# Optimization experiments

Measured on AMD Instinct MI355X. Metric: run time of the kernel, lower is better.

## Reference

```python
import jax, jax.numpy as jnp
import numpy as np
from jax import lax

B, C, H, W = 2, 256, 64, 64
CI = C // 2           # inter_channels = 128
CH = CI // 2          # key/query channels = 64
EPS = 1e-5


def conv1x1(x, w, b):
    # x: [B,C,H,W], w: [O,C], b: [O]
    return jnp.einsum('oc,bchw->bohw', w, x) + b[None, :, None, None]


def bn(x, g, be, m, v):
    inv = (g / jnp.sqrt(v + EPS))[None, :, None, None]
    return (x - m[None, :, None, None]) * inv + be[None, :, None, None]


def setup_inputs() -> dict:
    key = jax.random.key(0)
    ks = jax.random.split(key, 40)
    r = lambda i, shape, sc=0.05: jax.random.normal(ks[i], shape, dtype=jnp.float32) * sc
    u = lambda i, shape: jax.random.uniform(ks[i], shape, dtype=jnp.float32, minval=0.5, maxval=1.5)
    return {
        'q': jax.random.normal(ks[0], (B, C, H, W), dtype=jnp.float32),
        's': jax.random.normal(ks[1], (B, C, H, W), dtype=jnp.float32),
        'scale': jnp.full((1,), 0.3, dtype=jnp.float32),
        'w_v': r(2, (CI, C)), 'b_v': r(3, (CI,)),
        'w_k1': r(4, (CH, C)), 'b_k1': r(5, (CH,)),
        'w_q1': r(6, (CH, C)), 'b_q1': r(7, (CH,)),
        'w_k2': r(8, (CH, C)), 'b_k2': r(9, (CH,)),
        'w_q2': r(10, (CH, C)), 'b_q2': r(11, (CH,)),
        'w_ts': r(12, (CI, C)), 'b_ts': r(13, (CI,)),
        'g_ts': u(14, (CI,)), 'be_ts': r(15, (CI,)), 'm_ts': r(16, (CI,)), 'v_ts': u(17, (CI,)),
        'w_tq': r(18, (CI, C)), 'b_tq': r(19, (CI,)),
        'g_tq': u(20, (CI,)), 'be_tq': r(21, (CI,)), 'm_tq': r(22, (CI,)), 'v_tq': u(23, (CI,)),
        'w_cat': r(24, (CI, 2 * CI, 3, 3)),
        'g_cat': u(25, (CI,)), 'be_cat': r(26, (CI,)), 'm_cat': r(27, (CI,)), 'v_cat': u(28, (CI,)),
    }


def reference(q, s, scale, w_v, b_v, w_k1, b_k1, w_q1, b_q1, w_k2, b_k2, w_q2, b_q2,
              w_ts, b_ts, g_ts, be_ts, m_ts, v_ts,
              w_tq, b_tq, g_tq, be_tq, m_tq, v_tq,
              w_cat, g_cat, be_cat, m_cat, v_cat):
    b_, _, h, w = q.shape
    n = h * w
    # values: [B, N, CI]
    v_q = conv1x1(q, w_v, b_v).reshape(b_, CI, n).transpose(0, 2, 1)
    v_s = conv1x1(s, w_v, b_v).reshape(b_, CI, n).transpose(0, 2, 1)
    # concatenated keys/queries: [B, CI, N]
    k_x = jnp.concatenate([conv1x1(q, w_k1, b_k1), conv1x1(s, w_k2, b_k2)], axis=1).reshape(b_, CI, n)
    q_x = jnp.concatenate([conv1x1(q, w_q1, b_q1), conv1x1(s, w_q2, b_q2)], axis=1).reshape(b_, CI, n)
    # affinity: [B, N, N]
    A_s = jnp.einsum('bcn,bcm->bnm', k_x, q_x)
    attn_s = jax.nn.softmax(A_s, axis=-1)
    attn_q = jax.nn.softmax(jnp.transpose(A_s, (0, 2, 1)), axis=-1)
    # p_s: [B, N, CI] -> [B, CI, H, W]
    p_s = jnp.einsum('bnm,bmc->bnc', attn_s, v_s).transpose(0, 2, 1).reshape(b_, CI, h, w)
    s_t = bn(conv1x1(s, w_ts, b_ts), g_ts, be_ts, m_ts, v_ts)
    q_t = bn(conv1x1(q, w_tq, b_tq), g_tq, be_tq, m_tq, v_tq)
    E_s = scale[0] * p_s + s_t
    q_s_ = jnp.einsum('bnm,bmc->bnc', attn_q, v_q).transpose(0, 2, 1).reshape(b_, CI, h, w)
    E_q = scale[0] * q_s_ + q_t
    cat = jnp.concatenate([E_q, E_s], axis=1)
    conv = lax.conv_general_dilated(cat, w_cat, (1, 1), 'SAME',
                                    dimension_numbers=('NCHW', 'OIHW', 'NCHW'))
    cpam = jax.nn.relu(bn(conv, g_cat, be_cat, m_cat, v_cat))
    return (cpam, E_q, E_s)
```

## Files before the change

### kernel.cpp

```cpp
#include <hip/hip_runtime.h>
#include <hip/hip_bf16.h>

#define NPIX 4096
#define NCH  256
#define CI   128
#define EPS  1e-5f
#define SOFF 20.0f

typedef unsigned short u16;
typedef __attribute__((ext_vector_type(8))) short short8;
typedef __attribute__((ext_vector_type(4))) float f32x4;

__device__ __forceinline__ float bfu2f(u16 u) {
    union { unsigned int i; float f; } x; x.i = ((unsigned int)u) << 16; return x.f;
}
__device__ __forceinline__ u16 f2bfu(float f) {
    union { float ff; unsigned int i; } x; x.ff = f;
    unsigned int r = x.i + 0x7FFFu + ((x.i >> 16) & 1u);
    return (u16)(r >> 16);
}

__device__ __forceinline__ void gload16(const u16* g, u16* l) {
    __builtin_amdgcn_global_load_lds(
        (const __attribute__((address_space(1))) unsigned int*)g,
        (__attribute__((address_space(3))) unsigned int*)l,
        16, 0, 0);
}

__global__ __launch_bounds__(256) void prep_kernel(
    const float* __restrict__ w_v,
    const float* __restrict__ w_k1, const float* __restrict__ w_q1,
    const float* __restrict__ w_k2, const float* __restrict__ w_q2,
    const float* __restrict__ w_ts, const float* __restrict__ w_tq,
    u16* __restrict__ Wbf,
    const float* __restrict__ w_cat, u16* __restrict__ wT)
{
    const int bx = blockIdx.x;
    if (bx < 768) {
        int idx = bx * 256 + threadIdx.x;
        int src = idx / 98304;
        int r   = idx - src * 98304;
        int o   = r >> 8, c = r & 255;
        float v;
        if (o < 128)      v = w_v[(size_t)o * 256 + c];
        else if (o < 192) v = (src ? w_k2 : w_k1)[(size_t)(o - 128) * 256 + c];
        else if (o < 256) v = (src ? w_q2 : w_q1)[(size_t)(o - 192) * 256 + c];
        else              v = (src ? w_ts : w_tq)[(size_t)(o - 256) * 256 + c];
        Wbf[idx] = f2bfu(v);
    } else {
        int co = bx - 768;
        const float* srcb = w_cat + (size_t)co * 2304;
        u16* dstb = wT + (size_t)co * 2304;
        for (int t = threadIdx.x; t < 2304; t += 256) {
            int ic = t / 9, tap = t - ic * 9;
            dstb[tap * 256 + ic] = f2bfu(srcb[t]);
        }
    }
}

__global__ __launch_bounds__(256) void proj2_kernel(
    const float* __restrict__ xq, const float* __restrict__ xs,
    const u16* __restrict__ Wbf,
    const float* __restrict__ b_v,
    const float* __restrict__ b_k1, const float* __restrict__ b_q1,
    const float* __restrict__ b_k2, const float* __restrict__ b_q2,
    const float* __restrict__ b_ts, const float* __restrict__ g_ts,
    const float* __restrict__ be_ts, const float* __restrict__ m_ts,
    const float* __restrict__ v_ts,
    const float* __restrict__ b_tq, const float* __restrict__ g_tq,
    const float* __restrict__ be_tq, const float* __restrict__ m_tq,
    const float* __restrict__ v_tq,
    u16* __restrict__ kT, u16* __restrict__ qT,
    u16* __restrict__ vq, u16* __restrict__ vs,
    u16* __restrict__ tq, u16* __restrict__ ts)
{
    __shared__ u16 Xs[64 * 264];
    __shared__ u16 KQ[64 * 136];

    const int tid  = threadIdx.x;
    const int lane = tid & 63;
    const int wid  = tid >> 6;
    const int l16  = lane & 15;
    const int quad = lane >> 4;

    const int n0  = blockIdx.x * 64;
    const int bz  = blockIdx.z;
    const int b   = bz >> 1, src = bz & 1;

    const float* xg = (src ? xs : xq) + (size_t)b * NCH * NPIX + n0;
    #pragma unroll
    for (int k0 = 0; k0 < 64; k0 += 16) {
        float v[16];
        #pragma unroll
        for (int k = 0; k < 16; ++k) {
            int idx = tid + (k0 + k) * 256;
            int c = idx >> 6, n = idx & 63;
            v[k] = xg[(size_t)c * NPIX + n];
        }
        #pragma unroll
        for (int k = 0; k < 16; ++k) {
            int idx = tid + (k0 + k) * 256;
            int c = idx >> 6, n = idx & 63;
            Xs[n * 264 + c] = f2bfu(v[k]);
        }
    }
    __syncthreads();

    const u16* W = Wbf + (size_t)src * 384 * 256;
    const int o0w = wid * 96;
    const float* bk = src ? b_k2 : b_k1;
    const float* bq = src ? b_q2 : b_q1;
    const float* bt = src ? b_ts : b_tq;

    f32x4 acc[24];
    #pragma unroll
    for (int ot = 0; ot < 6; ++ot) {
        int ob = o0w + ot * 16 + quad * 4;
        const float* bp;
        if (ob < 128)      bp = b_v + ob;
        else if (ob < 192) bp = bk + (ob - 128);
        else if (ob < 256) bp = bq + (ob - 192);
        else               bp = bt + (ob - 256);
        float4 b4 = *(const float4*)bp;
        f32x4 iv = (f32x4){b4.x, b4.y, b4.z, b4.w};
        #pragma unroll
        for (int pt = 0; pt < 4; ++pt) acc[ot * 4 + pt] = iv;
    }

    #pragma unroll
    for (int kc = 0; kc < 8; ++kc) {
        short8 bfr[4];
        #pragma unroll
        for (int pt = 0; pt < 4; ++pt)
            bfr[pt] = *(const short8*)&Xs[(pt * 16 + l16) * 264 + kc * 32 + quad * 8];
        #pragma unroll
        for (int ot = 0; ot < 6; ++ot) {
            short8 a = *(const short8*)&W[(size_t)(o0w + ot * 16 + l16) * 256 + kc * 32 + quad * 8];
            #pragma unroll
            for (int pt = 0; pt < 4; ++pt)
                acc[ot * 4 + pt] = __builtin_amdgcn_mfma_f32_16x16x32_bf16(a, bfr[pt], acc[ot * 4 + pt], 0, 0, 0);
        }
    }

    #pragma unroll
    for (int ot = 0; ot < 6; ++ot) {
        int ob = o0w + ot * 16;
        #pragma unroll
        for (int pt = 0; pt < 4; ++pt) {
            int px = pt * 16 + l16;
            f32x4 v4 = acc[ot * 4 + pt];
            if (ob < 128) {
                u16* dst = src ? vs : vq;
                #pragma unroll
                for (int r = 0; r < 4; ++r)
                    dst[((size_t)b * CI + ob + quad * 4 + r) * NPIX + n0 + px] = f2bfu(v4[r]);
            } else if (ob < 256) {
                int colb = (ob < 192) ? (ob - 128) : (64 + ob - 192);
                #pragma unroll
                for (int r = 0; r < 4; ++r)
                    KQ[px * 136 + colb + quad * 4 + r] = f2bfu(v4[r]);
            } else {
                const float* g  = src ? g_ts  : g_tq;
                const float* be = src ? be_ts : be_tq;
                const float* mm = src ? m_ts  : m_tq;
                const float* vv = src ? v_ts  : v_tq;
                u16* dst = src ? ts : tq;
                #pragma unroll
                for (int r = 0; r < 4; ++r) {
                    int oc = ob - 256 + quad * 4 + r;
                    float inv = g[oc] * rsqrtf(vv[oc] + EPS);
                    dst[((size_t)b * CI + oc) * NPIX + n0 + px] =
                        f2bfu((v4[r] - mm[oc]) * inv + be[oc]);
                }
            }
        }
    }
    __syncthreads();

    const int chb = src ? 64 : 0;
    #pragma unroll
    for (int u = 0; u < 4; ++u) {
        int idx = tid + u * 256;
        int px = idx >> 4, oct = idx & 15;
        uint4 val = *(const uint4*)&KQ[px * 136 + oct * 8];
        if (oct < 8)
            *(uint4*)&kT[((size_t)b * NPIX + n0 + px) * CI + chb + oct * 8] = val;
        else
            *(uint4*)&qT[((size_t)b * NPIX + n0 + px) * CI + chb + (oct - 8) * 8] = val;
    }
}

#define AKS_OFF 0
#define AVT_OFF 16384
#define APS_OFF 32768
#define ASMEM_U16 37376

__global__ __launch_bounds__(256) void attn_kernel(
    const u16* __restrict__ kT, const u16* __restrict__ qT,
    const u16* __restrict__ vq, const u16* __restrict__ vs,
    u16* __restrict__ Opart, float* __restrict__ Lpart, int nseg)
{
    __shared__ __align__(16) u16 smem[ASMEM_U16];
    u16* Ps = smem + APS_OFF;

    const int tid  = threadIdx.x;
    const int lane = tid & 63;
    const int wid  = tid >> 6;
    const int l16  = lane & 15;
    const int quad = lane >> 4;
    const int strip = wid * 16;

    const int nt = blockIdx.x;
    const int n0 = nt * 64;
    const int at = blockIdx.y;
    const int z  = blockIdx.z;
    const int b  = z / nseg;
    const int seg = z - b * nseg;

    const u16* Qg = at ? qT : kT;
    const u16* Kg = at ? kT : qT;
    const u16* Vg = at ? vq : vs;

    short8 qf[4];
    {
        const u16* Qb = Qg + ((size_t)b * NPIX + n0 + strip + l16) * CI;
        #pragma unroll
        for (int kc = 0; kc < 4; ++kc)
            qf[kc] = *(const short8*)&Qb[kc * 32 + quad * 8];
    }

    f32x4 o[8];
    #pragma unroll
    for (int ct = 0; ct < 8; ++ct) o[ct] = (f32x4){0.f, 0.f, 0.f, 0.f};
    float L = 0.f;

    const u16* KgB = Kg + (size_t)b * NPIX * CI;
    const u16* VgB = Vg + (size_t)b * CI * NPIX;

    const int mt0 = seg * (64 / nseg);
    const int mt1 = mt0 + (64 / nseg);

    #define ISSUE_TILE(buf, m0_)                                              \
    {                                                                         \
        u16* kb_ = smem + AKS_OFF + (buf) * 8192;                             \
        u16* vb_ = smem + AVT_OFF + (buf) * 8192;                             \
        _Pragma("unroll")                                                     \
        for (int k = 0; k < 4; ++k) {                                         \
            int sb  = k * 256 + wid * 64;                                     \
            int idx = sb + lane;                                              \
            int row = idx >> 4, segp = idx & 15;                              \
            int segg = segp ^ (row & 15);                                     \
            gload16(KgB + (size_t)((m0_) + row) * CI + segg * 8, kb_ + sb * 8); \
        }                                                                     \
        _Pragma("unroll")                                                     \
        for (int k = 0; k < 4; ++k) {                                         \
            int sb  = k * 256 + wid * 64;                                     \
            int idx = sb + lane;                                              \
            int c = idx >> 3, sgp = idx & 7;                                  \
            int sgg = sgp ^ (c & 7);                                          \
            gload16(VgB + (size_t)c * NPIX + (m0_) + sgg * 8, vb_ + sb * 8);  \
        }                                                                     \
    }

    int cur = 0;
    ISSUE_TILE(0, mt0 * 64);

    for (int mt = mt0; mt < mt1; ++mt) {
        __syncthreads();
        if (mt + 1 < mt1) ISSUE_TILE(1 - cur, (mt + 1) * 64);

        const u16* Ks = smem + AKS_OFF + cur * 8192;
        const u16* Vt = smem + AVT_OFF + cur * 8192;

        f32x4 sv[4];
        #pragma unroll
        for (int m2 = 0; m2 < 4; ++m2) {
            f32x4 c = (f32x4){0.f, 0.f, 0.f, 0.f};
            #pragma unroll
            for (int kc = 0; kc < 4; ++kc) {
                int s = kc * 4 + quad;
                short8 kf = *(const short8*)&Ks[(m2 * 16 + l16) * 128 + ((s ^ l16) * 8)];
                c = __builtin_amdgcn_mfma_f32_16x16x32_bf16(kf, qf[kc], c, 0, 0, 0);
            }
            sv[m2] = c;
        }

        float Lsum = 0.f;
        u16* myPs = Ps + (strip + l16) * 72;
        #pragma unroll
        for (int m2 = 0; m2 < 4; ++m2) {
            float p0 = __expf(sv[m2][0] - SOFF);
            float p1 = __expf(sv[m2][1] - SOFF);
            float p2 = __expf(sv[m2][2] - SOFF);
            float p3 = __expf(sv[m2][3] - SOFF);
            Lsum += (p0 + p1) + (p2 + p3);
            ushort4 pk;
            pk.x = f2bfu(p0); pk.y = f2bfu(p1);
            pk.z = f2bfu(p2); pk.w = f2bfu(p3);
            *(ushort4*)&myPs[m2 * 16 + quad * 4] = pk;
        }
        Lsum += __shfl_xor(Lsum, 16);
        Lsum += __shfl_xor(Lsum, 32);
        L += Lsum;

        short8 ap[2];
        #pragma unroll
        for (int kc = 0; kc < 2; ++kc)
            ap[kc] = *(const short8*)&Ps[(strip + l16) * 72 + kc * 32 + quad * 8];
        #pragma unroll
        for (int ct = 0; ct < 8; ++ct) {
            #pragma unroll
            for (int kc = 0; kc < 2; ++kc) {
                int s = kc * 4 + quad;
                short8 bv = *(const short8*)&Vt[(ct * 16 + l16) * 64 + ((s ^ (l16 & 7)) * 8)];
                o[ct] = __builtin_amdgcn_mfma_f32_16x16x32_bf16(ap[kc], bv, o[ct], 0, 0, 0);
            }
        }
        cur ^= 1;
    }

    const size_t tile = (((size_t)(at * 2 + b) * 64 + nt) * nseg + seg);
    u16* Ob = Opart + tile * 8192;
    #pragma unroll
    for (int r = 0; r < 4; ++r) {
        int row = strip + quad * 4 + r;
        #pragma unroll
        for (int ct = 0; ct < 8; ++ct)
            Ob[row * 128 + ct * 16 + l16] = f2bfu(o[ct][r]);
    }
    if (quad == 0)
        Lpart[tile * 64 + strip + l16] = L;
    #undef ISSUE_TILE
}

__global__ __launch_bounds__(256) void attn_combine_kernel(
    const u16* __restrict__ Opart, const float* __restrict__ Lpart,
    const u16* __restrict__ tq, const u16* __restrict__ ts,
    const float* __restrict__ scale_p,
    float* __restrict__ out, u16* __restrict__ Ebf, int nseg)
{
    __shared__ float Of[128 * 68];
    __shared__ float invL[64];

    const int tid = threadIdx.x;
    const int nt = blockIdx.x;
    const int n0 = nt * 64;
    const int at = blockIdx.y;
    const int b  = blockIdx.z;

    const u16* Tg = at ? tq : ts;
    float* outE   = out + (size_t)(at ? 1 : 2) * 1048576;
    const int ch0 = at ? 0 : 128;
    const size_t tbase = ((size_t)(at * 2 + b) * 64 + nt) * nseg;

    if (tid < 64) {
        float Lg = 0.f;
        for (int s = 0; s < nseg; ++s) Lg += Lpart[(tbase + s) * 64 + tid];
        invL[tid] = 1.f / Lg;
    }
    __syncthreads();

    #pragma unroll
    for (int k = 0; k < 4; ++k) {
        int idx = tid + k * 256;
        int row = idx >> 4, oct = idx & 15;
        float m[8] = {0.f, 0.f, 0.f, 0.f, 0.f, 0.f, 0.f, 0.f};
        for (int s = 0; s < nseg; ++s) {
            union { uint4 v; u16 u[8]; } pk;
            pk.v = *(const uint4*)&Opart[(tbase + s) * 8192 + row * 128 + oct * 8];
            #pragma unroll
            for (int j = 0; j < 8; ++j) m[j] += bfu2f(pk.u[j]);
        }
        float w = invL[row];
        #pragma unroll
        for (int j = 0; j < 8; ++j)
            Of[(oct * 8 + j) * 68 + row] = m[j] * w;
    }
    __syncthreads();

    float scale = *scale_p;
    const u16* Tb = Tg + (size_t)b * CI * NPIX + n0;
    float* Ob = outE + (size_t)b * CI * NPIX + n0;
    for (int idx = tid; idx < 128 * 64; idx += 256) {
        int c = idx >> 6, r = idx & 63;
        float v = scale * Of[c * 68 + r] + bfu2f(Tb[(size_t)c * NPIX + r]);
        Ob[(size_t)c * NPIX + r] = v;
        Ebf[((size_t)b * NPIX + n0 + r) * NCH + ch0 + c] = f2bfu(v);
    }
}

#define CXT_STR 40

__global__ __launch_bounds__(256) void conv_kernel(
    const u16* __restrict__ Ebf,
    const u16* __restrict__ wT,
    const float* __restrict__ g_cat, const float* __restrict__ be_cat,
    const float* __restrict__ m_cat, const float* __restrict__ v_cat,
    float* __restrict__ out)
{
    __shared__ u16 XtW[4][3 * 34 * CXT_STR];

    const int tid  = threadIdx.x;
    const int lane = tid & 63;
    const int wid  = tid >> 6;
    const int l16  = lane & 15;
    const int quad = lane >> 4;

    const int h    = blockIdx.x;
    const int coff = blockIdx.y * 32;
    const int b    = blockIdx.z;

    const int cot = wid >> 1;
    const int pxt = (wid & 1) * 2;
    const int gc0 = pxt * 16 - 1;

    f32x4 acc[2];
    #pragma unroll
    for (int j = 0; j < 2; ++j) acc[j] = (f32x4){0.f, 0.f, 0.f, 0.f};

    const u16* Eb = Ebf + (size_t)b * NPIX * NCH;
    u16* Xw = &XtW[wid][0];
    const int cobase = coff + cot * 16 + l16;

    for (int icc = 0; icc < 8; ++icc) {
        const int ic0 = icc * 32;

        short8 wfrag[9];
        #pragma unroll
        for (int tap = 0; tap < 9; ++tap)
            wfrag[tap] = *(const short8*)&wT[((size_t)cobase * 9 + tap) * 256 + ic0 + quad * 8];

        for (int u = lane; u < 408; u += 64) {
            int part = u & 3, xe = u >> 2;
            int dh = xe / 34, x = xe - dh * 34;
            int gr = h + dh - 1, gc = gc0 + x;
            uint4 val = make_uint4(0u, 0u, 0u, 0u);
            if ((unsigned)gr < 64u && (unsigned)gc < 64u)
                val = *(const uint4*)&Eb[((size_t)gr * 64 + gc) * NCH + ic0 + part * 8];
            *(uint4*)&Xw[(dh * 34 + x) * CXT_STR + part * 8] = val;
        }

        #pragma unroll
        for (int tap = 0; tap < 9; ++tap) {
            const int dh = tap / 3, dw = tap % 3;
            short8 bf[2];
            #pragma unroll
            for (int j = 0; j < 2; ++j) {
                int x = j * 16 + l16 + dw;
                bf[j] = *(const short8*)&Xw[(dh * 34 + x) * CXT_STR + quad * 8];
            }
            #pragma unroll
            for (int j = 0; j < 2; ++j)
                acc[j] = __builtin_amdgcn_mfma_f32_16x16x32_bf16(wfrag[tap], bf[j], acc[j], 0, 0, 0);
        }
    }

    #pragma unroll
    for (int r = 0; r < 4; ++r) {
        int co = coff + cot * 16 + quad * 4 + r;
        float inv = g_cat[co] * rsqrtf(v_cat[co] + EPS);
        float mm  = m_cat[co];
        float be  = be_cat[co];
        #pragma unroll
        for (int j = 0; j < 2; ++j) {
            int wcol = (pxt + j) * 16 + l16;
            float v = (acc[j][r] - mm) * inv + be;
            out[((size_t)b * CI + co) * NPIX + h * 64 + wcol] = fmaxf(v, 0.f);
        }
    }
}

extern "C" void kernel_launch(void* const* d_in, const int* in_sizes, int n_in,
                              void* d_out, int out_size, void* d_ws, size_t ws_size,
                              hipStream_t stream)
{
    const float* q     = (const float*)d_in[0];
    const float* s     = (const float*)d_in[1];
    const float* scale = (const float*)d_in[2];
    const float* w_v   = (const float*)d_in[3];
    const float* b_v   = (const float*)d_in[4];
    const float* w_k1  = (const float*)d_in[5];
    const float* b_k1  = (const float*)d_in[6];
    const float* w_q1  = (const float*)d_in[7];
    const float* b_q1  = (const float*)d_in[8];
    const float* w_k2  = (const float*)d_in[9];
    const float* b_k2  = (const float*)d_in[10];
    const float* w_q2  = (const float*)d_in[11];
    const float* b_q2  = (const float*)d_in[12];
    const float* w_ts  = (const float*)d_in[13];
    const float* b_ts  = (const float*)d_in[14];
    const float* g_ts  = (const float*)d_in[15];
    const float* be_ts = (const float*)d_in[16];
    const float* m_ts  = (const float*)d_in[17];
    const float* v_ts  = (const float*)d_in[18];
    const float* w_tq  = (const float*)d_in[19];
    const float* b_tq  = (const float*)d_in[20];
    const float* g_tq  = (const float*)d_in[21];
    const float* be_tq = (const float*)d_in[22];
    const float* m_tq  = (const float*)d_in[23];
    const float* v_tq  = (const float*)d_in[24];
    const float* w_cat = (const float*)d_in[25];
    const float* g_cat = (const float*)d_in[26];
    const float* be_cat= (const float*)d_in[27];
    const float* m_cat = (const float*)d_in[28];
    const float* v_cat = (const float*)d_in[29];

    float* out = (float*)d_out;
    u16* ws = (u16*)d_ws;
    const size_t SZ = (size_t)2 * CI * NPIX;
    u16* kT  = ws;
    u16* qT  = kT + SZ;
    u16* vq  = qT + SZ;
    u16* vs  = vq + SZ;
    u16* tq  = vs + SZ;
    u16* ts  = tq + SZ;
    u16* Wbf = ts + SZ;
    u16* B   = Wbf + 196608;
    u16* Ebf = B;
    u16* wTc = B + 2097152;
    u16* Opart = wTc + 294912;

    const size_t fixed_u16 = 6 * SZ + 196608 + 2097152 + 294912;
    int nseg = 1;
    {
        size_t need4 = (fixed_u16 + (size_t)4 * 2097152) * 2 + (size_t)4 * 131072;
        size_t need2 = (fixed_u16 + (size_t)2 * 2097152) * 2 + (size_t)2 * 131072;
        if (ws_size >= need4)      nseg = 4;
        else if (ws_size >= need2) nseg = 2;
    }
    float* Lpart = (float*)(Opart + (size_t)nseg * 256 * 8192);

    dim3 blk(256);
    hipLaunchKernelGGL(prep_kernel, dim3(896), blk, 0, stream,
                       w_v, w_k1, w_q1, w_k2, w_q2, w_ts, w_tq, Wbf, w_cat, wTc);
    hipLaunchKernelGGL(proj2_kernel, dim3(64, 1, 4), blk, 0, stream,
                       q, s, Wbf, b_v, b_k1, b_q1, b_k2, b_q2,
                       b_ts, g_ts, be_ts, m_ts, v_ts,
                       b_tq, g_tq, be_tq, m_tq, v_tq,
                       kT, qT, vq, vs, tq, ts);
    hipLaunchKernelGGL(attn_kernel, dim3(64, 2, 2 * nseg), blk, 0, stream,
                       kT, qT, vq, vs, Opart, Lpart, nseg);
    hipLaunchKernelGGL(attn_combine_kernel, dim3(64, 2, 2), blk, 0, stream,
                       Opart, Lpart, tq, ts, scale, out, Ebf, nseg);
    hipLaunchKernelGGL(conv_kernel, dim3(64, 4, 2), blk, 0, stream,
                       Ebf, wTc, g_cat, be_cat, m_cat, v_cat, out);
}
```

Measured before the change: 248.4 us.

## Halve attention KV tile to 32 keys to raise occupancy, add setprio and packed bf16 cvt

Shrinks the per-iteration key/value tile in the attention kernel from 64 to 32 rows, halving LDS use so four blocks can fit per CU (launch bounds set to 4). The V swizzle is reworked for the narrower 32-wide layout, and MFMA sections are wrapped in s_setprio to favour matrix issue. The f32-to-bf16 conversion of probabilities now uses the hardware packed convert instruction instead of manual rounding. The trade-off is twice as many loop iterations and barriers per block, with less work per barrier.

```diff
diff --git a/kernel.cpp b/kernel.cpp
--- a/kernel.cpp
+++ b/kernel.cpp
@@ -191,11 +191,11 @@
 }
 
 #define AKS_OFF 0
-#define AVT_OFF 16384
-#define APS_OFF 32768
-#define ASMEM_U16 37376
-
-__global__ __launch_bounds__(256) void attn_kernel(
+#define AVT_OFF 8192
+#define APS_OFF 16384
+#define ASMEM_U16 18944
+
+__global__ __launch_bounds__(256, 4) void attn_kernel(
     const u16* __restrict__ kT, const u16* __restrict__ qT,
     const u16* __restrict__ vq, const u16* __restrict__ vs,
     u16* __restrict__ Opart, float* __restrict__ Lpart, int nseg)
@@ -237,15 +237,15 @@
     const u16* KgB = Kg + (size_t)b * NPIX * CI;
     const u16* VgB = Vg + (size_t)b * CI * NPIX;
 
-    const int mt0 = seg * (64 / nseg);
-    const int mt1 = mt0 + (64 / nseg);
+    const int mt0 = seg * (128 / nseg);
+    const int mt1 = mt0 + (128 / nseg);
 
     #define ISSUE_TILE(buf, m0_)                                              \
     {                                                                         \
-        u16* kb_ = smem + AKS_OFF + (buf) * 8192;                             \
-        u16* vb_ = smem + AVT_OFF + (buf) * 8192;                             \
+        u16* kb_ = smem + AKS_OFF + (buf) * 4096;                             \
+        u16* vb_ = smem + AVT_OFF + (buf) * 4096;                             \
         _Pragma("unroll")                                                     \
-        for (int k = 0; k < 4; ++k) {                                         \
+        for (int k = 0; k < 2; ++k) {                                         \
             int sb  = k * 256 + wid * 64;                                     \
             int idx = sb + lane;                                              \
             int row = idx >> 4, segp = idx & 15;                              \
@@ -253,28 +253,29 @@
             gload16(KgB + (size_t)((m0_) + row) * CI + segg * 8, kb_ + sb * 8); \
         }                                                                     \
         _Pragma("unroll")                                                     \
-        for (int k = 0; k < 4; ++k) {                                         \
+        for (int k = 0; k < 2; ++k) {                                         \
             int sb  = k * 256 + wid * 64;                                     \
             int idx = sb + lane;                                              \
-            int c = idx >> 3, sgp = idx & 7;                                  \
-            int sgg = sgp ^ (c & 7);                                          \
+            int c = idx >> 2, sgp = idx & 3;                                  \
+            int sgg = sgp ^ ((c ^ (c >> 2)) & 3);                             \
             gload16(VgB + (size_t)c * NPIX + (m0_) + sgg * 8, vb_ + sb * 8);  \
         }                                                                     \
     }
 
     int cur = 0;
-    ISSUE_TILE(0, mt0 * 64);
+    ISSUE_TILE(0, mt0 * 32);
 
     for (int mt = mt0; mt < mt1; ++mt) {
         __syncthreads();
-        if (mt + 1 < mt1) ISSUE_TILE(1 - cur, (mt + 1) * 64);
-
-        const u16* Ks = smem + AKS_OFF + cur * 8192;
-        const u16* Vt = smem + AVT_OFF + cur * 8192;
-
-        f32x4 sv[4];
-        #pragma unroll
-        for (int m2 = 0; m2 < 4; ++m2) {
+        if (mt + 1 < mt1) ISSUE_TILE(1 - cur, (mt + 1) * 32);
+
+        const u16* Ks = smem + AKS_OFF + cur * 4096;
+        const u16* Vt = smem + AVT_OFF + cur * 4096;
+
+        f32x4 sv[2];
+        __builtin_amdgcn_s_setprio(1);
+        #pragma unroll
+        for (int m2 = 0; m2 < 2; ++m2) {
             f32x4 c = (f32x4){0.f, 0.f, 0.f, 0.f};
             #pragma unroll
             for (int kc = 0; kc < 4; ++kc) {
@@ -284,38 +285,37 @@
             }
             sv[m2] = c;
         }
+        __builtin_amdgcn_s_setprio(0);
 
         float Lsum = 0.f;
-        u16* myPs = Ps + (strip + l16) * 72;
-        #pragma unroll
-        for (int m2 = 0; m2 < 4; ++m2) {
+        u16* myPs = Ps + (strip + l16) * 40;
+        #pragma unroll
+        for (int m2 = 0; m2 < 2; ++m2) {
             float p0 = __expf(sv[m2][0] - SOFF);
             float p1 = __expf(sv[m2][1] - SOFF);
             float p2 = __expf(sv[m2][2] - SOFF);
             float p3 = __expf(sv[m2][3] - SOFF);
             Lsum += (p0 + p1) + (p2 + p3);
-            ushort4 pk;
-            pk.x = f2bfu(p0); pk.y = f2bfu(p1);
-            pk.z = f2bfu(p2); pk.w = f2bfu(p3);
-            *(ushort4*)&myPs[m2 * 16 + quad * 4] = pk;
+            unsigned int r0, r1;
+            asm("v_cvt_pk_bf16_f32 %0, %1, %2" : "=v"(r0) : "v"(p0), "v"(p1));
+            asm("v_cvt_pk_bf16_f32 %0, %1, %2" : "=v"(r1) : "v"(p2), "v"(p3));
+            uint2 pk; pk.x = r0; pk.y = r1;
+            *(uint2*)&myPs[m2 * 16 + quad * 4] = pk;
         }
         Lsum += __shfl_xor(Lsum, 16);
         Lsum += __shfl_xor(Lsum, 32);
         L += Lsum;
 
-        short8 ap[2];
-        #pragma unroll
-        for (int kc = 0; kc < 2; ++kc)
-            ap[kc] = *(const short8*)&Ps[(strip + l16) * 72 + kc * 32 + quad * 8];
+        short8 ap = *(const short8*)&Ps[(strip + l16) * 40 + quad * 8];
+        __builtin_amdgcn_s_setprio(1);
         #pragma unroll
         for (int ct = 0; ct < 8; ++ct) {
-            #pragma unroll
-            for (int kc = 0; kc < 2; ++kc) {
-                int s = kc * 4 + quad;
-                short8 bv = *(const short8*)&Vt[(ct * 16 + l16) * 64 + ((s ^ (l16 & 7)) * 8)];
-                o[ct] = __builtin_amdgcn_mfma_f32_16x16x32_bf16(ap[kc], bv, o[ct], 0, 0, 0);
-            }
-        }
+            int cc = ct * 16 + l16;
+            int fc = (cc ^ (cc >> 2)) & 3;
+            short8 bv = *(const short8*)&Vt[cc * 32 + ((quad ^ fc) * 8)];
+            o[ct] = __builtin_amdgcn_mfma_f32_16x16x32_bf16(ap, bv, o[ct], 0, 0, 0);
+        }
+        __builtin_amdgcn_s_setprio(0);
         cur ^= 1;
     }
 
```

Result: faster. 241.4 us (-2.8%).
